# Optimization experiments

Measured on AMD Instinct MI355X. Metric: run time of the kernel, lower is better.

Reference implementation:

```python
import jax, jax.numpy as jnp
import numpy as np

B, S, H, D = 2, 2048, 16, 64
HID = H * D
NEG_INF = -10000.0

def setup_inputs() -> dict:
    key = jax.random.key(0)
    ks = jax.random.split(key, 4)
    std = 0.02
    return {
        'x': jax.random.normal(ks[0], (B, S, HID), dtype=jnp.float32),
        'mask': jnp.ones((B, S), dtype=jnp.int32),
        'Wq': jax.random.normal(ks[1], (HID, HID), dtype=jnp.float32) * std,
        'bq': jnp.zeros((HID,), dtype=jnp.float32),
        'Wk': jax.random.normal(ks[2], (HID, HID), dtype=jnp.float32) * std,
        'bk': jnp.zeros((HID,), dtype=jnp.float32),
        'Wv': jax.random.normal(ks[3], (HID, HID), dtype=jnp.float32) * std,
        'bv': jnp.zeros((HID,), dtype=jnp.float32),
    }

def reference(x, mask, Wq, bq, Wk, bk, Wv, bv):
    b, s, _ = x.shape
    def split_heads(t):  # [b,s,HID] -> [b,H,s,D]
        return t.reshape(b, s, H, D).transpose(0, 2, 1, 3)
    q = split_heads(x @ Wq + bq)
    k = split_heads(x @ Wk + bk)
    v = split_heads(x @ Wv + bv)
    scores = jnp.einsum('bhqd,bhkd->bhqk', q, k) / jnp.sqrt(jnp.float32(D))
    # additive padding mask: [b,1,1,s] broadcast over query positions and heads
    adder = (1.0 - mask.astype(scores.dtype))[:, None, None, :] * NEG_INF
    probs = jax.nn.softmax(scores + adder, axis=-1)
    ctx = jnp.einsum('bhqk,bhkd->bhqd', probs, v)  # [b,H,s,D]
    return ctx.transpose(0, 2, 1, 3).reshape(b, s, HID)
```

## Files before the change

kernel.cpp:

```cpp
#include <hip/hip_runtime.h>
#include <cstddef>

constexpr int Bc = 2, Sc = 2048, Hc = 16, Dc = 64, HIDc = 1024;
#define NEG_INF -10000.0f
#define LOG2E 1.44269504088896340736f

typedef _Float16 half8  __attribute__((ext_vector_type(8)));
typedef _Float16 half4  __attribute__((ext_vector_type(4)));
typedef float   floatx4 __attribute__((ext_vector_type(4)));

__device__ __forceinline__ void gload_lds16(const void* g, void* l) {
    __builtin_amdgcn_global_load_lds(
        (const __attribute__((address_space(1))) unsigned int*)g,
        (__attribute__((address_space(3))) unsigned int*)l, 16, 0, 0);
}

__global__ __launch_bounds__(256) void cvt_x_kernel(const float* __restrict__ x,
                                                    _Float16* __restrict__ xh) {
    int i = (blockIdx.x * 256 + threadIdx.x) * 8;
    float4 a = *(const float4*)(x + i);
    float4 b = *(const float4*)(x + i + 4);
    half8 h;
    h[0] = (_Float16)a.x; h[1] = (_Float16)a.y; h[2] = (_Float16)a.z; h[3] = (_Float16)a.w;
    h[4] = (_Float16)b.x; h[5] = (_Float16)b.y; h[6] = (_Float16)b.z; h[7] = (_Float16)b.w;
    *(half8*)(xh + i) = h;
}

__global__ __launch_bounds__(256) void cvt_w_kernel(const float* __restrict__ Wq,
                                                    const float* __restrict__ Wk,
                                                    const float* __restrict__ Wv,
                                                    _Float16* __restrict__ Wt) {
    const float* W = (blockIdx.z == 0) ? Wq : (blockIdx.z == 1) ? Wk : Wv;
    _Float16* out = Wt + (size_t)blockIdx.z * HIDc * HIDc;
    __shared__ _Float16 T[64][65];
    const int t = threadIdx.x;
    const int kb = blockIdx.x * 64, nb = blockIdx.y * 64;
    const int r = t >> 2, c4 = (t & 3) * 16;
    #pragma unroll
    for (int i = 0; i < 16; i += 4) {
        float4 a = *(const float4*)(W + (size_t)(kb + r) * HIDc + nb + c4 + i);
        T[c4 + i + 0][r] = (_Float16)a.x;
        T[c4 + i + 1][r] = (_Float16)a.y;
        T[c4 + i + 2][r] = (_Float16)a.z;
        T[c4 + i + 3][r] = (_Float16)a.w;
    }
    __syncthreads();
    const int n = t >> 2, k4 = (t & 3) * 16;
    half8 o0, o1;
    #pragma unroll
    for (int j = 0; j < 8; ++j) { o0[j] = T[n][k4 + j]; o1[j] = T[n][k4 + 8 + j]; }
    *(half8*)(out + (size_t)(nb + n) * HIDc + kb + k4)     = o0;
    *(half8*)(out + (size_t)(nb + n) * HIDc + kb + k4 + 8) = o1;
}

__global__ __launch_bounds__(256, 3) void proj_kernel(
    const _Float16* __restrict__ xh, const _Float16* __restrict__ Wt,
    const float* __restrict__ bq, const float* __restrict__ bk, const float* __restrict__ bv,
    _Float16* __restrict__ qw, _Float16* __restrict__ kw, _Float16* __restrict__ vt)
{
    const int z = blockIdx.z;
    const _Float16* Wz = Wt + (size_t)z * HIDc * HIDc;
    const float* bias = (z == 0) ? bq : (z == 1) ? bk : bv;

    __shared__ __align__(16) _Float16 SM[2][2][128 * 32];

    const int t = threadIdx.x;
    const int lane = t & 63, w = t >> 6;
    const int quad = lane >> 4, l16 = lane & 15;
    const int m0 = blockIdx.y * 128, n0 = blockIdx.x * 128;
    const int wm = (w >> 1) * 64, wn = (w & 1) * 64;

    const int srl = lane >> 2;
    const int ssl = (lane & 3) ^ ((lane >> 3) & 3);

    floatx4 acc[4][4];
    #pragma unroll
    for (int mb = 0; mb < 4; ++mb)
        #pragma unroll
        for (int nb = 0; nb < 4; ++nb) acc[mb][nb] = floatx4{0.f, 0.f, 0.f, 0.f};

    auto stage = [&](int buf, int kt) {
        #pragma unroll
        for (int j = 0; j < 2; ++j) {
            const int rb = (w + 4 * j) * 16;
            gload_lds16(xh + (size_t)(m0 + rb + srl) * HIDc + kt + ssl * 8,
                        &SM[buf][0][rb * 32]);
            gload_lds16(Wz + (size_t)(n0 + rb + srl) * HIDc + kt + ssl * 8,
                        &SM[buf][1][rb * 32]);
        }
    };

    stage(0, 0);
    __syncthreads();

    const int sA = (quad ^ ((l16 >> 1) & 3)) * 8;

    #pragma unroll 2
    for (int it = 0; it < HIDc / 32; ++it) {
        const int cur = it & 1;
        const int kn = (it + 1 < HIDc / 32) ? (it + 1) * 32 : 0;
        stage(cur ^ 1, kn);

        half8 af[4], bf[4];
        #pragma unroll
        for (int mb = 0; mb < 4; ++mb)
            af[mb] = *(const half8*)(&SM[cur][0][(wm + mb * 16 + l16) * 32 + sA]);
        #pragma unroll
        for (int nb = 0; nb < 4; ++nb)
            bf[nb] = *(const half8*)(&SM[cur][1][(wn + nb * 16 + l16) * 32 + sA]);
        #pragma unroll
        for (int mb = 0; mb < 4; ++mb)
            #pragma unroll
            for (int nb = 0; nb < 4; ++nb)
                acc[mb][nb] = __builtin_amdgcn_mfma_f32_16x16x32_f16(
                    af[mb], bf[nb], acc[mb][nb], 0, 0, 0);
        __syncthreads();
    }

    if (z == 2) {
        _Float16* T = (_Float16*)SM;
        const int bI0 = m0 >> 11, m0s = m0 & (Sc - 1);
        #pragma unroll
        for (int p = 0; p < 2; ++p) {
            __syncthreads();
            if ((w & 1) == p) {
                #pragma unroll
                for (int nb = 0; nb < 4; ++nb) {
                    const int n = nb * 16 + l16;
                    const float bi = bias[n0 + p * 64 + n];
                    #pragma unroll
                    for (int mb = 0; mb < 4; ++mb) {
                        half4 h4;
                        #pragma unroll
                        for (int r = 0; r < 4; ++r)
                            h4[r] = (_Float16)(acc[mb][nb][r] + bi);
                        *(half4*)(T + n * 136 + wm + mb * 16 + quad * 4) = h4;
                    }
                }
            }
            __syncthreads();
            const int n = t >> 2;
            const int N = n0 + p * 64 + n, hh = N >> 6, d = N & 63;
            _Float16* vrow = vt + (((size_t)(bI0 * Hc + hh)) * Dc + d) * Sc + m0s;
            #pragma unroll
            for (int j = 0; j < 4; ++j) {
                const int c = (t & 3) * 32 + j * 8;
                *(uint4*)(vrow + c) = *(const uint4*)(T + n * 136 + c);
            }
        }
        return;
    }
    #pragma unroll
    for (int nb = 0; nb < 4; ++nb) {
        const int N = n0 + wn + nb * 16 + l16;
        const float bi = bias[N];
        const int h = N >> 6, d = N & 63;
        #pragma unroll
        for (int mb = 0; mb < 4; ++mb) {
            #pragma unroll
            for (int r = 0; r < 4; ++r) {
                const int M = m0 + wm + mb * 16 + quad * 4 + r;
                const int bI = M >> 11, s = M & (Sc - 1);
                const float v = acc[mb][nb][r] + bi;
                if (z == 0)
                    qw[(((size_t)(bI * Hc + h)) * Sc + s) * Dc + d] =
                        (_Float16)(v * (0.125f * LOG2E));
                else
                    kw[(((size_t)(bI * Hc + h)) * Sc + s) * Dc + d] = (_Float16)v;
            }
        }
    }
}

__global__ __launch_bounds__(256, 2) void attn_kernel(
    const _Float16* __restrict__ qw, const _Float16* __restrict__ kw,
    const _Float16* __restrict__ vt, const int* __restrict__ mask,
    float* __restrict__ out)
{
    __shared__ __align__(16) float adder[Sc];
    __shared__ __align__(16) _Float16 Ks[2][64][72];
    __shared__ __align__(16) _Float16 Vs[2][64][72];

    const int t = threadIdx.x;
    const int lane = t & 63, w = t >> 6;
    const int quad = lane >> 4, l16 = lane & 15;
    const int bh = blockIdx.y;
    const int bI = bh >> 4, h = bh & 15;

    const _Float16* Qp = qw + (size_t)bh * Sc * Dc;
    const _Float16* Kp = kw + (size_t)bh * Sc * Dc;
    const _Float16* Vp = vt + (size_t)bh * Dc * Sc;

    const int srow = t >> 3;
    const int scol = (t & 7) * 8;
    const int m7 = t & 7;
    const int vc0 = 32 * (m7 & 1) + 4 * (m7 >> 1);

    {
        const int4* mp = (const int4*)(mask + bI * Sc);
        #pragma unroll
        for (int i = 0; i < 2; ++i) {
            int4 m4 = mp[t * 2 + i];
            int base = (t * 2 + i) * 4;
            adder[base + 0] = (1.0f - (float)m4.x) * (NEG_INF * LOG2E);
            adder[base + 1] = (1.0f - (float)m4.y) * (NEG_INF * LOG2E);
            adder[base + 2] = (1.0f - (float)m4.z) * (NEG_INF * LOG2E);
            adder[base + 3] = (1.0f - (float)m4.w) * (NEG_INF * LOG2E);
        }
    }
    #pragma unroll
    for (int hf = 0; hf < 2; ++hf) {
        const int row = srow + 32 * hf;
        uint4 kv = *(const uint4*)(Kp + (size_t)row * Dc + scol);
        uint4 vv = *(const uint4*)(Vp + (size_t)row * Sc + scol);
        *(uint4*)(&Ks[0][row][scol]) = kv;
        *(uint2*)(&Vs[0][row][vc0])      = make_uint2(vv.x, vv.y);
        *(uint2*)(&Vs[0][row][vc0 + 16]) = make_uint2(vv.z, vv.w);
    }

    const int qrow = blockIdx.x * 128 + w * 32;
    half8 aq[2][2];
    #pragma unroll
    for (int s = 0; s < 2; ++s)
        #pragma unroll
        for (int hh = 0; hh < 2; ++hh)
            aq[s][hh] = *(const half8*)(Qp + (size_t)(qrow + 16 * s + l16) * Dc
                                        + hh * 32 + quad * 8);

    floatx4 o[2][4], osum[2];
    #pragma unroll
    for (int s = 0; s < 2; ++s) {
        osum[s] = floatx4{0.f, 0.f, 0.f, 0.f};
        #pragma unroll
        for (int db = 0; db < 4; ++db) o[s][db] = floatx4{0.f, 0.f, 0.f, 0.f};
    }
    const half8 ones8 = {(_Float16)1.f, (_Float16)1.f, (_Float16)1.f, (_Float16)1.f,
                         (_Float16)1.f, (_Float16)1.f, (_Float16)1.f, (_Float16)1.f};

    __syncthreads();

    #pragma unroll 2
    for (int it = 0; it < Sc / 64; ++it) {
        const int cur = it & 1;
        const int kt = it * 64;
        const int ktn = (it + 1 < Sc / 64) ? kt + 64 : 0;
        uint4 kstg[2], vstg[2];
        #pragma unroll
        for (int hf = 0; hf < 2; ++hf) {
            const int row = srow + 32 * hf;
            kstg[hf] = *(const uint4*)(Kp + (size_t)(ktn + row) * Dc + scol);
            vstg[hf] = *(const uint4*)(Vp + (size_t)row * Sc + ktn + scol);
        }

        half8 kb[4][2];
        #pragma unroll
        for (int nb = 0; nb < 4; ++nb)
            #pragma unroll
            for (int hh = 0; hh < 2; ++hh)
                kb[nb][hh] = *(const half8*)(&Ks[cur][nb * 16 + l16][hh * 32 + quad * 8]);

        half8 vb8[2][4];
        #pragma unroll
        for (int db = 0; db < 4; ++db)
            #pragma unroll
            for (int a = 0; a < 2; ++a)
                vb8[a][db] = *(const half8*)(&Vs[cur][db * 16 + l16][quad * 16 + a * 8]);

        floatx4 st[2][4];
        __builtin_amdgcn_s_setprio(1);
        #pragma unroll
        for (int nb = 0; nb < 4; ++nb) {
            const floatx4 adv = *(const floatx4*)(&adder[kt + nb * 16 + quad * 4]);
            #pragma unroll
            for (int s = 0; s < 2; ++s) {
                floatx4 x0 = __builtin_amdgcn_mfma_f32_16x16x32_f16(kb[nb][0], aq[s][0], adv, 0, 0, 0);
                st[s][nb]  = __builtin_amdgcn_mfma_f32_16x16x32_f16(kb[nb][1], aq[s][1], x0, 0, 0, 0);
            }
        }
        __builtin_amdgcn_s_setprio(0);

        half4 pa[2][4];
        #pragma unroll
        for (int s = 0; s < 2; ++s)
            #pragma unroll
            for (int nb = 0; nb < 4; ++nb)
                #pragma unroll
                for (int r = 0; r < 4; ++r)
                    pa[s][nb][r] = (_Float16)__builtin_amdgcn_exp2f(st[s][nb][r]);

        __builtin_amdgcn_s_setprio(1);
        #pragma unroll
        for (int s = 0; s < 2; ++s)
            #pragma unroll
            for (int a = 0; a < 2; ++a) {
                const half8 pf = __builtin_shufflevector(
                    pa[s][2 * a], pa[s][2 * a + 1], 0, 1, 2, 3, 4, 5, 6, 7);
                osum[s] = __builtin_amdgcn_mfma_f32_16x16x32_f16(pf, ones8, osum[s], 0, 0, 0);
                #pragma unroll
                for (int db = 0; db < 4; ++db)
                    o[s][db] = __builtin_amdgcn_mfma_f32_16x16x32_f16(
                        pf, vb8[a][db], o[s][db], 0, 0, 0);
            }
        __builtin_amdgcn_s_setprio(0);

        #pragma unroll
        for (int hf = 0; hf < 2; ++hf) {
            const int row = srow + 32 * hf;
            *(uint4*)(&Ks[cur ^ 1][row][scol]) = kstg[hf];
            const uint4 vv = vstg[hf];
            *(uint2*)(&Vs[cur ^ 1][row][vc0])      = make_uint2(vv.x, vv.y);
            *(uint2*)(&Vs[cur ^ 1][row][vc0 + 16]) = make_uint2(vv.z, vv.w);
        }
        __syncthreads();
    }

    float* op = out + (size_t)bI * Sc * HIDc + h * Dc;
    #pragma unroll
    for (int s = 0; s < 2; ++s)
        #pragma unroll
        for (int r = 0; r < 4; ++r) {
            const float inv = __builtin_amdgcn_rcpf(osum[s][r]);
            const int q = qrow + 16 * s + quad * 4 + r;
            #pragma unroll
            for (int db = 0; db < 4; ++db)
                op[(size_t)q * HIDc + db * 16 + l16] = o[s][db][r] * inv;
        }
}

extern "C" void kernel_launch(void* const* d_in, const int* in_sizes, int n_in,
                              void* d_out, int out_size, void* d_ws, size_t ws_size,
                              hipStream_t stream) {
    const float* x    = (const float*)d_in[0];
    const int*   mask = (const int*)  d_in[1];
    const float* Wq   = (const float*)d_in[2];
    const float* bq   = (const float*)d_in[3];
    const float* Wk   = (const float*)d_in[4];
    const float* bk   = (const float*)d_in[5];
    const float* Wv   = (const float*)d_in[6];
    const float* bv   = (const float*)d_in[7];
    float* out = (float*)d_out;

    char* ws = (char*)d_ws;
    _Float16* xh = (_Float16*)(ws);
    _Float16* Wt = (_Float16*)(ws + (size_t)8  * 1024 * 1024);
    _Float16* qw = (_Float16*)(ws + (size_t)14 * 1024 * 1024);
    _Float16* kw = (_Float16*)(ws + (size_t)22 * 1024 * 1024);
    _Float16* vt = (_Float16*)(ws + (size_t)30 * 1024 * 1024);

    cvt_x_kernel<<<(Bc * Sc * HIDc) / (256 * 8), 256, 0, stream>>>(x, xh);
    cvt_w_kernel<<<dim3(HIDc / 64, HIDc / 64, 3), 256, 0, stream>>>(Wq, Wk, Wv, Wt);
    proj_kernel<<<dim3(HIDc / 128, (Bc * Sc) / 128, 3), 256, 0, stream>>>(
        xh, Wt, bq, bk, bv, qw, kw, vt);
    attn_kernel<<<dim3(Sc / 128, Bc * Hc), 256, 0, stream>>>(qw, kw, vt, mask, out);
}
```

Before: 166.1 us.

## Software-pipeline attention: overlap next tile's QK^T with previous PV and exp

Restructures the attention inner loop into a two-stage software pipeline. Each step computes QK^T for the current key tile while issuing the PV MFMAs for the previous tile's probabilities, with V fragments and packed probabilities held in ping-pong registers. The exp and convert work moves after the MFMAs, so VALU work can overlap matrix work. It also packs exp results with cvt_pkrtz, which rounds toward zero instead of to nearest, and remaps block indices so that consecutive blocks spread across heads. The cost is higher register pressure under launch_bounds(256,2) and a small precision change from the rounding mode.

```diff
diff --git a/kernel.cpp b/kernel.cpp
--- a/kernel.cpp
+++ b/kernel.cpp
@@ -7,6 +7,8 @@
 
 typedef _Float16 half8  __attribute__((ext_vector_type(8)));
 typedef _Float16 half4  __attribute__((ext_vector_type(4)));
+typedef __fp16   f16x2  __attribute__((ext_vector_type(2)));
+typedef __fp16   f16x4  __attribute__((ext_vector_type(4)));
 typedef float   floatx4 __attribute__((ext_vector_type(4)));
 
 __device__ __forceinline__ void gload_lds16(const void* g, void* l) {
@@ -172,6 +174,77 @@
     }
 }
 
+#define ATTN_STEP(IT, CUR, VBOUT, PAOUT, VBIN, PAIN, DOPV) do {               \
+    const int kt_ = (IT) * 64;                                                \
+    const int ktn_ = ((IT) + 1 < Sc / 64) ? kt_ + 64 : 0;                     \
+    uint4 kstg_[2], vstg_[2];                                                 \
+    _Pragma("unroll")                                                         \
+    for (int hf = 0; hf < 2; ++hf) {                                          \
+        const int row = srow + 32 * hf;                                       \
+        kstg_[hf] = *(const uint4*)(Kp + (size_t)(ktn_ + row) * Dc + scol);   \
+        vstg_[hf] = *(const uint4*)(Vp + (size_t)row * Sc + ktn_ + scol);     \
+    }                                                                         \
+    half8 kb_[4][2];                                                          \
+    _Pragma("unroll")                                                         \
+    for (int nb = 0; nb < 4; ++nb)                                            \
+        _Pragma("unroll")                                                     \
+        for (int hh = 0; hh < 2; ++hh)                                        \
+            kb_[nb][hh] = *(const half8*)(&Ks[CUR][nb * 16 + l16][hh * 32 + quad * 8]); \
+    _Pragma("unroll")                                                         \
+    for (int db = 0; db < 4; ++db)                                            \
+        _Pragma("unroll")                                                     \
+        for (int a = 0; a < 2; ++a)                                           \
+            VBOUT[a][db] = *(const half8*)(&Vs[CUR][db * 16 + l16][quad * 16 + a * 8]); \
+    floatx4 st_[2][4];                                                        \
+    __builtin_amdgcn_s_setprio(1);                                            \
+    _Pragma("unroll")                                                         \
+    for (int nb = 0; nb < 4; ++nb) {                                          \
+        const floatx4 adv = *(const floatx4*)(&adder[kt_ + nb * 16 + quad * 4]); \
+        _Pragma("unroll")                                                     \
+        for (int s = 0; s < 2; ++s) {                                         \
+            floatx4 x0 = __builtin_amdgcn_mfma_f32_16x16x32_f16(kb_[nb][0], aq[s][0], adv, 0, 0, 0); \
+            st_[s][nb] = __builtin_amdgcn_mfma_f32_16x16x32_f16(kb_[nb][1], aq[s][1], x0, 0, 0, 0);  \
+        }                                                                     \
+    }                                                                         \
+    if (DOPV) {                                                               \
+        _Pragma("unroll")                                                     \
+        for (int s = 0; s < 2; ++s)                                           \
+            _Pragma("unroll")                                                 \
+            for (int a = 0; a < 2; ++a) {                                     \
+                const half8 pf = __builtin_shufflevector(                     \
+                    PAIN[s][2 * a], PAIN[s][2 * a + 1], 0, 1, 2, 3, 4, 5, 6, 7); \
+                osum[s] = __builtin_amdgcn_mfma_f32_16x16x32_f16(pf, ones8, osum[s], 0, 0, 0); \
+                _Pragma("unroll")                                             \
+                for (int db = 0; db < 4; ++db)                                \
+                    o[s][db] = __builtin_amdgcn_mfma_f32_16x16x32_f16(        \
+                        pf, VBIN[a][db], o[s][db], 0, 0, 0);                  \
+            }                                                                 \
+    }                                                                         \
+    __builtin_amdgcn_s_setprio(0);                                            \
+    _Pragma("unroll")                                                         \
+    for (int s = 0; s < 2; ++s)                                               \
+        _Pragma("unroll")                                                     \
+        for (int nb = 0; nb < 4; ++nb) {                                      \
+            const f16x2 lo_ = __builtin_amdgcn_cvt_pkrtz(                     \
+                __builtin_amdgcn_exp2f(st_[s][nb][0]),                        \
+                __builtin_amdgcn_exp2f(st_[s][nb][1]));                       \
+            const f16x2 hi_ = __builtin_amdgcn_cvt_pkrtz(                     \
+                __builtin_amdgcn_exp2f(st_[s][nb][2]),                        \
+                __builtin_amdgcn_exp2f(st_[s][nb][3]));                       \
+            const f16x4 pk_ = __builtin_shufflevector(lo_, hi_, 0, 1, 2, 3);  \
+            PAOUT[s][nb] = __builtin_bit_cast(half4, pk_);                    \
+        }                                                                     \
+    _Pragma("unroll")                                                         \
+    for (int hf = 0; hf < 2; ++hf) {                                          \
+        const int row = srow + 32 * hf;                                       \
+        *(uint4*)(&Ks[(CUR) ^ 1][row][scol]) = kstg_[hf];                     \
+        const uint4 vv = vstg_[hf];                                           \
+        *(uint2*)(&Vs[(CUR) ^ 1][row][vc0])      = make_uint2(vv.x, vv.y);    \
+        *(uint2*)(&Vs[(CUR) ^ 1][row][vc0 + 16]) = make_uint2(vv.z, vv.w);    \
+    }                                                                         \
+    __syncthreads();                                                          \
+} while (0)
+
 __global__ __launch_bounds__(256, 2) void attn_kernel(
     const _Float16* __restrict__ qw, const _Float16* __restrict__ kw,
     const _Float16* __restrict__ vt, const int* __restrict__ mask,
@@ -184,7 +257,11 @@
     const int t = threadIdx.x;
     const int lane = t & 63, w = t >> 6;
     const int quad = lane >> 4, l16 = lane & 15;
-    const int bh = blockIdx.y;
+
+    const int flat = blockIdx.y * 16 + blockIdx.x;
+    const int idx = flat >> 3;
+    const int bh = (flat & 7) * 4 + (idx & 3);
+    const int qt = idx >> 2;
     const int bI = bh >> 4, h = bh & 15;
 
     const _Float16* Qp = qw + (size_t)bh * Sc * Dc;
@@ -218,7 +295,7 @@
         *(uint2*)(&Vs[0][row][vc0 + 16]) = make_uint2(vv.z, vv.w);
     }
 
-    const int qrow = blockIdx.x * 128 + w * 32;
+    const int qrow = qt * 128 + w * 32;
     half8 aq[2][2];
     #pragma unroll
     for (int s = 0; s < 2; ++s)
@@ -237,82 +314,33 @@
     const half8 ones8 = {(_Float16)1.f, (_Float16)1.f, (_Float16)1.f, (_Float16)1.f,
                          (_Float16)1.f, (_Float16)1.f, (_Float16)1.f, (_Float16)1.f};
 
+    half8 vbA[2][4], vbB[2][4];
+    half4 paA[2][4], paB[2][4];
+
     __syncthreads();
 
-    #pragma unroll 2
-    for (int it = 0; it < Sc / 64; ++it) {
-        const int cur = it & 1;
-        const int kt = it * 64;
-        const int ktn = (it + 1 < Sc / 64) ? kt + 64 : 0;
-        uint4 kstg[2], vstg[2];
-        #pragma unroll
-        for (int hf = 0; hf < 2; ++hf) {
-            const int row = srow + 32 * hf;
-            kstg[hf] = *(const uint4*)(Kp + (size_t)(ktn + row) * Dc + scol);
-            vstg[hf] = *(const uint4*)(Vp + (size_t)row * Sc + ktn + scol);
-        }
-
-        half8 kb[4][2];
-        #pragma unroll
-        for (int nb = 0; nb < 4; ++nb)
-            #pragma unroll
-            for (int hh = 0; hh < 2; ++hh)
-                kb[nb][hh] = *(const half8*)(&Ks[cur][nb * 16 + l16][hh * 32 + quad * 8]);
-
-        half8 vb8[2][4];
-        #pragma unroll
-        for (int db = 0; db < 4; ++db)
-            #pragma unroll
-            for (int a = 0; a < 2; ++a)
-                vb8[a][db] = *(const half8*)(&Vs[cur][db * 16 + l16][quad * 16 + a * 8]);
-
-        floatx4 st[2][4];
-        __builtin_amdgcn_s_setprio(1);
-        #pragma unroll
-        for (int nb = 0; nb < 4; ++nb) {
-            const floatx4 adv = *(const floatx4*)(&adder[kt + nb * 16 + quad * 4]);
-            #pragma unroll
-            for (int s = 0; s < 2; ++s) {
-                floatx4 x0 = __builtin_amdgcn_mfma_f32_16x16x32_f16(kb[nb][0], aq[s][0], adv, 0, 0, 0);
-                st[s][nb]  = __builtin_amdgcn_mfma_f32_16x16x32_f16(kb[nb][1], aq[s][1], x0, 0, 0, 0);
-            }
-        }
-        __builtin_amdgcn_s_setprio(0);
-
-        half4 pa[2][4];
-        #pragma unroll
-        for (int s = 0; s < 2; ++s)
-            #pragma unroll
-            for (int nb = 0; nb < 4; ++nb)
-                #pragma unroll
-                for (int r = 0; r < 4; ++r)
-                    pa[s][nb][r] = (_Float16)__builtin_amdgcn_exp2f(st[s][nb][r]);
-
-        __builtin_amdgcn_s_setprio(1);
-        #pragma unroll
-        for (int s = 0; s < 2; ++s)
-            #pragma unroll
-            for (int a = 0; a < 2; ++a) {
-                const half8 pf = __builtin_shufflevector(
-                    pa[s][2 * a], pa[s][2 * a + 1], 0, 1, 2, 3, 4, 5, 6, 7);
-                osum[s] = __builtin_amdgcn_mfma_f32_16x16x32_f16(pf, ones8, osum[s], 0, 0, 0);
-                #pragma unroll
-                for (int db = 0; db < 4; ++db)
-                    o[s][db] = __builtin_amdgcn_mfma_f32_16x16x32_f16(
-                        pf, vb8[a][db], o[s][db], 0, 0, 0);
-            }
-        __builtin_amdgcn_s_setprio(0);
-
-        #pragma unroll
-        for (int hf = 0; hf < 2; ++hf) {
-            const int row = srow + 32 * hf;
-            *(uint4*)(&Ks[cur ^ 1][row][scol]) = kstg[hf];
-            const uint4 vv = vstg[hf];
-            *(uint2*)(&Vs[cur ^ 1][row][vc0])      = make_uint2(vv.x, vv.y);
-            *(uint2*)(&Vs[cur ^ 1][row][vc0 + 16]) = make_uint2(vv.z, vv.w);
-        }
-        __syncthreads();
-    }
+    ATTN_STEP(0, 0, vbA, paA, vbB, paB, 0);
+    for (int j = 0; j < 15; ++j) {
+        const int itb = 2 * j;
+        ATTN_STEP(itb + 1, 1, vbB, paB, vbA, paA, 1);
+        ATTN_STEP(itb + 2, 0, vbA, paA, vbB, paB, 1);
+    }
+    ATTN_STEP(31, 1, vbB, paB, vbA, paA, 1);
+
+    __builtin_amdgcn_s_setprio(1);
+    #pragma unroll
+    for (int s = 0; s < 2; ++s)
+        #pragma unroll
+        for (int a = 0; a < 2; ++a) {
+            const half8 pf = __builtin_shufflevector(
+                paB[s][2 * a], paB[s][2 * a + 1], 0, 1, 2, 3, 4, 5, 6, 7);
+            osum[s] = __builtin_amdgcn_mfma_f32_16x16x32_f16(pf, ones8, osum[s], 0, 0, 0);
+            #pragma unroll
+            for (int db = 0; db < 4; ++db)
+                o[s][db] = __builtin_amdgcn_mfma_f32_16x16x32_f16(
+                    pf, vbB[a][db], o[s][db], 0, 0, 0);
+        }
+    __builtin_amdgcn_s_setprio(0);
 
     float* op = out + (size_t)bI * Sc * HIDc + h * Dc;
     #pragma unroll
```

Measured after the change: 161.8 us. -2.6%, faster.
